# Optimization experiments

Measured on AMD Instinct MI355X. Metric: run time of the kernel, lower is better.

The kernel has to match this reference:

```python
import jax, jax.numpy as jnp
import numpy as np

E = 1024
H = 16
D = E // H  # 64
S = 2048
B = 4


def setup_inputs() -> dict:
    key = jax.random.key(0)
    ks = jax.random.split(key, 9)
    scale = 1.0 / np.sqrt(E)
    inp = {"x": jax.random.normal(ks[0], (S, B, E), dtype=jnp.float32)}
    for i, name in enumerate(["q", "k", "v", "o"]):
        inp[f"W{name}"] = jax.random.uniform(ks[1 + 2 * i], (E, E), dtype=jnp.float32, minval=-scale, maxval=scale)
        inp[f"b{name}"] = jax.random.uniform(ks[2 + 2 * i], (E,), dtype=jnp.float32, minval=-scale, maxval=scale)
    return inp


def reference(x, Wq, bq, Wk, bk, Wv, bv, Wo, bo):
    s, b, e = x.shape
    # linear projections (torch Linear: x @ W.T + b), split into heads
    q = (x @ Wq.T + bq).reshape(s, b, H, D)
    k = (x @ Wk.T + bk).reshape(s, b, H, D)
    v = (x @ Wv.T + bv).reshape(s, b, H, D)
    # naive O(S^2) attention, scores: [S, B, H, S]
    scores = jnp.einsum('sbhd,tbhd->sbht', q, k) / np.sqrt(D).astype(np.float32)
    attn = jax.nn.softmax(scores, axis=3)
    # dropout p=0.0 (eval) -> identity
    out = jnp.einsum('sbht,tbhd->sbhd', attn, v).reshape(s, b, e)
    return out @ Wo.T + bo
```

## Files before the change

### kernel.cpp

```cpp
#include <hip/hip_runtime.h>
#include <hip/hip_bf16.h>

#define S_LEN 2048
#define BATCH 4
#define EMB   1024
#define NH    16
#define HD    64
#define NROW  8192

#define QSCALE 0.18033688011112043f

typedef __bf16 bf16x8 __attribute__((ext_vector_type(8)));
typedef float  f32x4  __attribute__((ext_vector_type(4)));

typedef __attribute__((address_space(3))) void lds_void;
typedef const __attribute__((address_space(1))) void gbl_void;
#define GLOAD_LDS16(g, l) __builtin_amdgcn_global_load_lds((gbl_void*)(g), (lds_void*)(l), 16, 0, 0)
#define MFMA16(a, b, c) __builtin_amdgcn_mfma_f32_16x16x32_bf16((a), (b), (c), 0, 0, 0)

#if __has_builtin(__builtin_amdgcn_exp2f)
#define EXP2(x) __builtin_amdgcn_exp2f(x)
#else
#define EXP2(x) __expf((x) * 0.6931471805599453f)
#endif

__global__ void cvt_all_kernel(const float* __restrict__ x,
                               const float* __restrict__ wq, const float* __restrict__ wk,
                               const float* __restrict__ wv, const float* __restrict__ wo,
                               __bf16* __restrict__ xb,
                               __bf16* __restrict__ qb, __bf16* __restrict__ kb,
                               __bf16* __restrict__ vb, __bf16* __restrict__ ob) {
    const int bid = blockIdx.x;
    const float* src;
    __bf16* dst;
    int i;
    if (bid < 8192) {
        src = x; dst = xb; i = bid * 256 + threadIdx.x;
    } else {
        const int w = (bid - 8192) >> 10;
        src = w == 0 ? wq : (w == 1 ? wk : (w == 2 ? wv : wo));
        dst = w == 0 ? qb : (w == 1 ? kb : (w == 2 ? vb : ob));
        i = ((bid - 8192) & 1023) * 256 + threadIdx.x;
    }
    float4 v = ((const float4*)src)[i];
    union { __bf16 h[4]; short4 s4; } u;
    u.h[0] = (__bf16)v.x; u.h[1] = (__bf16)v.y;
    u.h[2] = (__bf16)v.z; u.h[3] = (__bf16)v.w;
    ((short4*)dst)[i] = u.s4;
}

#define GSTEP(C, BT, VM, DOSTAGE) do {                                        \
    asm volatile("s_waitcnt vmcnt(" VM ")" ::: "memory");                     \
    __builtin_amdgcn_s_barrier();                                             \
    if (DOSTAGE) {                                                            \
        GLOAD_LDS16(gA0 + ((C) + 2) * 32, ldsA + (((BT) + 2) % 3) * 4096);    \
        GLOAD_LDS16(gA1 + ((C) + 2) * 32, ldsA + (((BT) + 2) % 3) * 4096 + 512); \
        GLOAD_LDS16(gW0 + ((C) + 2) * 32, ldsB + (((BT) + 2) % 3) * 4096);    \
        GLOAD_LDS16(gW1 + ((C) + 2) * 32, ldsB + (((BT) + 2) % 3) * 4096 + 512); \
    }                                                                         \
    bf16x8 af[4], bfr[4];                                                     \
    _Pragma("unroll")                                                         \
    for (int tt = 0; tt < 4; ++tt) {                                          \
        af[tt]  = *(const bf16x8*)(Ab + (BT) * 4096 + tt * 512);              \
        bfr[tt] = *(const bf16x8*)(Bb + (BT) * 4096 + tt * 512);              \
    }                                                                         \
    _Pragma("unroll")                                                         \
    for (int i = 0; i < 4; ++i)                                               \
        _Pragma("unroll")                                                     \
        for (int j = 0; j < 4; ++j)                                           \
            acc[i][j] = MFMA16(af[i], bfr[j], acc[i][j]);                     \
} while (0)

__global__ __launch_bounds__(256) void gemm_qkv_kernel(
    const __bf16* __restrict__ A,
    const __bf16* __restrict__ W0, const __bf16* __restrict__ W1,
    const __bf16* __restrict__ W2,
    const float* __restrict__ bi0, const float* __restrict__ bi1,
    const float* __restrict__ bi2,
    __bf16* __restrict__ Qo, __bf16* __restrict__ Ko, __bf16* __restrict__ Vo)
{
    __shared__ __align__(16) char SMEM[49152];
    __bf16* Asb = (__bf16*)SMEM;
    __bf16* Bsb = (__bf16*)(SMEM + 24576);

    const int flat = blockIdx.x;
    const int xcd = flat & 7, slot = flat >> 3;
    const int nB = slot >> 3;
    const int mB = (xcd << 3) | (slot & 7);
    const int which = nB >> 3;
    const __bf16* W = which == 0 ? W0 : (which == 1 ? W1 : W2);
    const float* bias = which == 0 ? bi0 : (which == 1 ? bi1 : bi2);
    __bf16* outb = which == 0 ? Qo : (which == 1 ? Ko : Vo);
    const int m0 = mB * 128;
    const int n0 = (nB & 7) * 128;

    const int lane = threadIdx.x & 63;
    const int wave = threadIdx.x >> 6;
    const int l15 = lane & 15;
    const int quad = lane >> 4;
    const int wm = (wave >> 1) * 64;
    const int wn = (wave & 1) * 64;

    const int c0 = wave * 128 + lane;
    const int c1 = c0 + 64;
    const int ar0 = c0 >> 2, ak0 = (((c0 & 3) ^ ((c0 >> 3) & 3))) * 8;
    const int ar1 = c1 >> 2, ak1 = (((c1 & 3) ^ ((c1 >> 3) & 3))) * 8;

    const __bf16* Ag = A + (size_t)m0 * EMB;
    const __bf16* Wg = W + (size_t)n0 * EMB;

    f32x4 acc[4][4];
#pragma unroll
    for (int i = 0; i < 4; ++i)
#pragma unroll
        for (int j = 0; j < 4; ++j) acc[i][j] = (f32x4){0.f, 0.f, 0.f, 0.f};

    const __bf16* gA0 = Ag + (size_t)ar0 * EMB + ak0;
    const __bf16* gA1 = Ag + (size_t)ar1 * EMB + ak1;
    const __bf16* gW0 = Wg + (size_t)ar0 * EMB + ak0;
    const __bf16* gW1 = Wg + (size_t)ar1 * EMB + ak1;
    __bf16* ldsA = Asb + wave * 1024;
    __bf16* ldsB = Bsb + wave * 1024;

    GLOAD_LDS16(gA0,      ldsA);
    GLOAD_LDS16(gA1,      ldsA + 512);
    GLOAD_LDS16(gW0,      ldsB);
    GLOAD_LDS16(gW1,      ldsB + 512);
    GLOAD_LDS16(gA0 + 32, ldsA + 4096);
    GLOAD_LDS16(gA1 + 32, ldsA + 4096 + 512);
    GLOAD_LDS16(gW0 + 32, ldsB + 4096);
    GLOAD_LDS16(gW1 + 32, ldsB + 4096 + 512);

    const int xr = (l15 >> 1) & 3;
    const __bf16* Ab = Asb + (wm + l15) * 32 + ((quad ^ xr) << 3);
    const __bf16* Bb = Bsb + (wn + l15) * 32 + ((quad ^ xr) << 3);

    for (int g = 0; g < 10; ++g) {
        GSTEP(0, 0, "4", 1);
        GSTEP(1, 1, "4", 1);
        GSTEP(2, 2, "4", 1);
        gA0 += 96; gA1 += 96; gW0 += 96; gW1 += 96;
    }
    GSTEP(0, 0, "4", 0);
    GSTEP(1, 1, "0", 0);

    __syncthreads();
    __bf16* epi = (__bf16*)SMEM + wave * 2304;
    float bv[4];
#pragma unroll
    for (int j = 0; j < 4; ++j) bv[j] = bias[n0 + wn + j * 16 + l15];
    const int hh = (n0 + wn) >> 6;

    if (which != 2) {
#pragma unroll
        for (int p = 0; p < 2; ++p) {
#pragma unroll
            for (int ih = 0; ih < 2; ++ih) {
                const int i = 2 * p + ih;
#pragma unroll
                for (int j = 0; j < 4; ++j)
#pragma unroll
                    for (int r = 0; r < 4; ++r) {
                        float v = acc[i][j][r] + bv[j];
                        if (which == 0) v *= QSCALE;
                        epi[(ih * 16 + quad * 4 + r) * 72 + j * 16 + l15] = (__bf16)v;
                    }
            }
#pragma unroll
            for (int ii = 0; ii < 4; ++ii) {
                const int rl = ii * 8 + (lane >> 3);
                bf16x8 row = *(const bf16x8*)(epi + rl * 72 + (lane & 7) * 8);
                const int m = m0 + wm + p * 32 + rl;
                const int b = m & 3, s = m >> 2;
                *(bf16x8*)(outb + ((size_t)(b * NH + hh) * S_LEN + s) * HD
                           + (lane & 7) * 8) = row;
            }
        }
    } else {
        const int sb = (m0 + wm) >> 2;
#pragma unroll
        for (int p = 0; p < 2; ++p) {
#pragma unroll
            for (int jh = 0; jh < 2; ++jh) {
                const int j = 2 * p + jh;
#pragma unroll
                for (int i = 0; i < 4; ++i)
#pragma unroll
                    for (int r = 0; r < 4; ++r) {
                        float v = acc[i][j][r] + bv[j];
                        epi[(jh * 16 + l15) * 72 + r * 16 + i * 4 + quad] = (__bf16)v;
                    }
            }
#pragma unroll
            for (int ii = 0; ii < 4; ++ii) {
                const int q = lane >> 1;
                bf16x8 row = *(const bf16x8*)(epi + q * 72 + ii * 16 + (lane & 1) * 8);
                const int d = p * 32 + q;
                *(bf16x8*)(outb + ((size_t)(ii * NH + hh) * HD + d) * S_LEN
                           + sb + (lane & 1) * 8) = row;
            }
        }
    }
}

__global__ __launch_bounds__(256) void gemm_out_kernel(
    const __bf16* __restrict__ A, const __bf16* __restrict__ W,
    const float* __restrict__ bias, float* __restrict__ outf)
{
    __shared__ __align__(16) char SMEM[49152];
    __bf16* Asb = (__bf16*)SMEM;
    __bf16* Bsb = (__bf16*)(SMEM + 24576);
    const int flat = blockIdx.x;
    const int xcd = flat & 7, slot = flat >> 3;
    const int nB = slot >> 3;
    const int mB = (xcd << 3) | (slot & 7);
    const int m0 = mB * 128;
    const int n0 = nB * 128;

    const int lane = threadIdx.x & 63;
    const int wave = threadIdx.x >> 6;
    const int l15 = lane & 15;
    const int quad = lane >> 4;
    const int wm = (wave >> 1) * 64;
    const int wn = (wave & 1) * 64;

    const int c0 = wave * 128 + lane;
    const int c1 = c0 + 64;
    const int ar0 = c0 >> 2, ak0 = (((c0 & 3) ^ ((c0 >> 3) & 3))) * 8;
    const int ar1 = c1 >> 2, ak1 = (((c1 & 3) ^ ((c1 >> 3) & 3))) * 8;

    const __bf16* Ag = A + (size_t)m0 * EMB;
    const __bf16* Wg = W + (size_t)n0 * EMB;

    f32x4 acc[4][4];
#pragma unroll
    for (int i = 0; i < 4; ++i)
#pragma unroll
        for (int j = 0; j < 4; ++j) acc[i][j] = (f32x4){0.f, 0.f, 0.f, 0.f};

    const __bf16* gA0 = Ag + (size_t)ar0 * EMB + ak0;
    const __bf16* gA1 = Ag + (size_t)ar1 * EMB + ak1;
    const __bf16* gW0 = Wg + (size_t)ar0 * EMB + ak0;
    const __bf16* gW1 = Wg + (size_t)ar1 * EMB + ak1;
    __bf16* ldsA = Asb + wave * 1024;
    __bf16* ldsB = Bsb + wave * 1024;

    GLOAD_LDS16(gA0,      ldsA);
    GLOAD_LDS16(gA1,      ldsA + 512);
    GLOAD_LDS16(gW0,      ldsB);
    GLOAD_LDS16(gW1,      ldsB + 512);
    GLOAD_LDS16(gA0 + 32, ldsA + 4096);
    GLOAD_LDS16(gA1 + 32, ldsA + 4096 + 512);
    GLOAD_LDS16(gW0 + 32, ldsB + 4096);
    GLOAD_LDS16(gW1 + 32, ldsB + 4096 + 512);

    const int xr = (l15 >> 1) & 3;
    const __bf16* Ab = Asb + (wm + l15) * 32 + ((quad ^ xr) << 3);
    const __bf16* Bb = Bsb + (wn + l15) * 32 + ((quad ^ xr) << 3);

    for (int g = 0; g < 10; ++g) {
        GSTEP(0, 0, "4", 1);
        GSTEP(1, 1, "4", 1);
        GSTEP(2, 2, "4", 1);
        gA0 += 96; gA1 += 96; gW0 += 96; gW1 += 96;
    }
    GSTEP(0, 0, "4", 0);
    GSTEP(1, 1, "0", 0);

#pragma unroll
    for (int j = 0; j < 4; ++j) {
        const int col = n0 + wn + j * 16 + l15;
        const float bv = bias[col];
#pragma unroll
        for (int i = 0; i < 4; ++i)
#pragma unroll
            for (int r = 0; r < 4; ++r) {
                const int m = m0 + wm + i * 16 + quad * 4 + r;
                outf[(size_t)m * EMB + col] = acc[i][j][r] + bv;
            }
    }
}

__global__ __launch_bounds__(256, 4) void attn_kernel(
    const __bf16* __restrict__ Q, const __bf16* __restrict__ Kp,
    const __bf16* __restrict__ Vt, __bf16* __restrict__ Ao)
{
    __shared__ __align__(16) __bf16 Ks[3][32 * 64];
    __shared__ __align__(16) __bf16 Vs[3][32 * 64];

    const int tid = threadIdx.x;
    const int lane = tid & 63;
    const int wave = tid >> 6;
    const int l15 = lane & 15;
    const int quad = lane >> 4;

    const int flat = blockIdx.y * gridDim.x + blockIdx.x;
    const int nf = (flat & 7) * 128 + (flat >> 3);
    const int bh = nf >> 4;
    const int b = bh >> 4, h = bh & 15;
    const int qw = (nf & 15) * 128 + wave * 32;

    const __bf16* Qb = Q  + (size_t)bh * S_LEN * HD;
    const __bf16* Kb = Kp + (size_t)bh * S_LEN * HD;
    const __bf16* Vb = Vt + (size_t)bh * HD * S_LEN;

    const int kr = tid >> 3;
    const int ks = ((tid & 7) ^ ((kr & 3) | (((kr >> 3) & 1) << 2))) * 8;
    const int vr = tid >> 2;
    const int vs = (((tid & 3) ^ ((tid >> 3) & 3))) * 8;

    bf16x8 qf[2][2];
#pragma unroll
    for (int mi = 0; mi < 2; ++mi)
#pragma unroll
        for (int kc = 0; kc < 2; ++kc)
            qf[mi][kc] = *(const bf16x8*)(Qb + (size_t)(qw + mi * 16 + l15) * HD
                                          + kc * 32 + quad * 8);

    bf16x8 ones;
#pragma unroll
    for (int i = 0; i < 8; ++i) ones[i] = (__bf16)1.0f;

    f32x4 acco[2][4], accl[2];
#pragma unroll
    for (int mi = 0; mi < 2; ++mi) {
        accl[mi] = (f32x4){0.f, 0.f, 0.f, 0.f};
#pragma unroll
        for (int nt = 0; nt < 4; ++nt) acco[mi][nt] = (f32x4){0.f, 0.f, 0.f, 0.f};
    }

    auto stageKV = [&](int t) {
        const int t0 = t * 32;
        GLOAD_LDS16(Kb + (size_t)(t0 + kr) * HD + ks, &Ks[t % 3][wave * 512]);
        GLOAD_LDS16(Vb + (size_t)vr * S_LEN + t0 + vs, &Vs[t % 3][wave * 512]);
    };
    stageKV(0);
    stageKV(1);

    const int ta = 8 * (l15 >> 2) + (l15 & 3);
    const int xk = (l15 & 3) | (((l15 >> 2) & 1) << 2);
    const int xv = (l15 >> 1) & 3;

    for (int it = 0; it < S_LEN / 32; ++it) {
        if (it < S_LEN / 32 - 1) asm volatile("s_waitcnt vmcnt(2)" ::: "memory");
        else                     asm volatile("s_waitcnt vmcnt(0)" ::: "memory");
        __builtin_amdgcn_s_barrier();
        if (it + 2 < S_LEN / 32) stageKV(it + 2);

        const __bf16* Kt = &Ks[it % 3][0];
        const __bf16* Vl = &Vs[it % 3][0];

        bf16x8 kfA[2], kfB[2], vf[4];
#pragma unroll
        for (int kc = 0; kc < 2; ++kc) {
            kfA[kc] = *(const bf16x8*)(Kt + ta * 64 + (((kc * 4 + quad) ^ xk) << 3));
            kfB[kc] = *(const bf16x8*)(Kt + (ta + 4) * 64 + (((kc * 4 + quad) ^ xk) << 3));
        }
#pragma unroll
        for (int nt = 0; nt < 4; ++nt)
            vf[nt] = *(const bf16x8*)(Vl + (nt * 16 + l15) * 32 + ((quad ^ xv) << 3));

        bf16x8 pf[2];
#pragma unroll
        for (int mi = 0; mi < 2; ++mi) {
            f32x4 sA = {0.f, 0.f, 0.f, 0.f}, sB = {0.f, 0.f, 0.f, 0.f};
            __builtin_amdgcn_s_setprio(1);
            sA = MFMA16(kfA[0], qf[mi][0], sA);
            sA = MFMA16(kfA[1], qf[mi][1], sA);
            sB = MFMA16(kfB[0], qf[mi][0], sB);
            sB = MFMA16(kfB[1], qf[mi][1], sB);
            __builtin_amdgcn_s_setprio(0);
            union { __bf16 hh[8]; bf16x8 v; } u;
#pragma unroll
            for (int r = 0; r < 4; ++r) {
                u.hh[r]     = (__bf16)EXP2(sA[r]);
                u.hh[4 + r] = (__bf16)EXP2(sB[r]);
            }
            pf[mi] = u.v;
        }
        __builtin_amdgcn_s_setprio(1);
#pragma unroll
        for (int mi = 0; mi < 2; ++mi)
            accl[mi] = MFMA16(pf[mi], ones, accl[mi]);
#pragma unroll
        for (int nt = 0; nt < 4; ++nt)
#pragma unroll
            for (int mi = 0; mi < 2; ++mi)
                acco[mi][nt] = MFMA16(pf[mi], vf[nt], acco[mi][nt]);
        __builtin_amdgcn_s_setprio(0);
    }

#pragma unroll
    for (int mi = 0; mi < 2; ++mi)
#pragma unroll
        for (int r = 0; r < 4; ++r) {
            const float inv = 1.0f / accl[mi][r];
            const int srow = qw + mi * 16 + quad * 4 + r;
            const int n = srow * BATCH + b;
#pragma unroll
            for (int nt = 0; nt < 4; ++nt)
                Ao[(size_t)n * EMB + h * 64 + nt * 16 + l15] =
                    (__bf16)(acco[mi][nt][r] * inv);
        }
}

extern "C" void kernel_launch(void* const* d_in, const int* in_sizes, int n_in,
                              void* d_out, int out_size, void* d_ws, size_t ws_size,
                              hipStream_t stream) {
    const float* x  = (const float*)d_in[0];
    const float* Wq = (const float*)d_in[1];
    const float* bq = (const float*)d_in[2];
    const float* Wk = (const float*)d_in[3];
    const float* bk = (const float*)d_in[4];
    const float* Wv = (const float*)d_in[5];
    const float* bv = (const float*)d_in[6];
    const float* Wo = (const float*)d_in[7];
    const float* bo = (const float*)d_in[8];
    float* out = (float*)d_out;

    char* ws = (char*)d_ws;
    const size_t xbf_sz = (size_t)NROW * EMB * 2;
    const size_t wbf_sz = (size_t)EMB * EMB * 2;
    const size_t qkv_sz = (size_t)BATCH * NH * S_LEN * HD * 2;
    __bf16* x_bf  = (__bf16*)ws;  ws += xbf_sz;
    __bf16* Wq_bf = (__bf16*)ws;  ws += wbf_sz;
    __bf16* Wk_bf = (__bf16*)ws;  ws += wbf_sz;
    __bf16* Wv_bf = (__bf16*)ws;  ws += wbf_sz;
    __bf16* Wo_bf = (__bf16*)ws;  ws += wbf_sz;
    __bf16* Qb    = (__bf16*)ws;  ws += qkv_sz;
    __bf16* Kb    = (__bf16*)ws;  ws += qkv_sz;
    __bf16* Vtb   = (__bf16*)ws;  ws += qkv_sz;
    __bf16* Aob   = (__bf16*)ws;  ws += qkv_sz;

    cvt_all_kernel<<<8192 + 4 * 1024, 256, 0, stream>>>(
        x, Wq, Wk, Wv, Wo, x_bf, Wq_bf, Wk_bf, Wv_bf, Wo_bf);

    gemm_qkv_kernel<<<64 * 24, 256, 0, stream>>>(x_bf, Wq_bf, Wk_bf, Wv_bf,
                                                 bq, bk, bv, Qb, Kb, Vtb);
    dim3 ag(S_LEN / 128, BATCH * NH);
    attn_kernel<<<ag, 256, 0, stream>>>(Qb, Kb, Vtb, Aob);
    gemm_out_kernel<<<(NROW / 128) * (EMB / 128), 256, 0, stream>>>(Aob, Wo_bf, bo, out);
}
```

Baseline: 251.8 us.

## Halve output GEMM M-tile to 64 rows and add LDS sync waits

The output projection GEMM now uses 64x128 tiles instead of 128x128, so the launch grows from 512 to 1024 blocks, each using less LDS and fewer accumulators. The aim is better occupancy and load balance across the CUs. The change also adds lgkmcnt(0) to the pipeline waits in the GEMM and attention loops and a __syncthreads between the two epilogue halves of the QKV kernel, which fixes LDS ordering hazards. In exchange the smaller tile re-reads the weight matrix from memory more often, and each block does less MFMA work per barrier.

```diff
diff --git a/kernel.cpp b/kernel.cpp
--- a/kernel.cpp
+++ b/kernel.cpp
@@ -50,7 +50,7 @@
 }
 
 #define GSTEP(C, BT, VM, DOSTAGE) do {                                        \
-    asm volatile("s_waitcnt vmcnt(" VM ")" ::: "memory");                     \
+    asm volatile("s_waitcnt vmcnt(" VM ") lgkmcnt(0)" ::: "memory");          \
     __builtin_amdgcn_s_barrier();                                             \
     if (DOSTAGE) {                                                            \
         GLOAD_LDS16(gA0 + ((C) + 2) * 32, ldsA + (((BT) + 2) % 3) * 4096);    \
@@ -71,6 +71,28 @@
             acc[i][j] = MFMA16(af[i], bfr[j], acc[i][j]);                     \
 } while (0)
 
+#define GSTEP2(C, BT, VM, DOSTAGE) do {                                       \
+    asm volatile("s_waitcnt vmcnt(" VM ") lgkmcnt(0)" ::: "memory");          \
+    __builtin_amdgcn_s_barrier();                                             \
+    if (DOSTAGE) {                                                            \
+        GLOAD_LDS16(gA0 + ((C) + 2) * 32, ldsA + (((BT) + 2) % 3) * 2048);    \
+        GLOAD_LDS16(gW0 + ((C) + 2) * 32, ldsB + (((BT) + 2) % 3) * 4096);    \
+        GLOAD_LDS16(gW1 + ((C) + 2) * 32, ldsB + (((BT) + 2) % 3) * 4096 + 512); \
+    }                                                                         \
+    bf16x8 af[2], bfr[4];                                                     \
+    _Pragma("unroll")                                                         \
+    for (int tt = 0; tt < 2; ++tt)                                            \
+        af[tt] = *(const bf16x8*)(Ab + (BT) * 2048 + tt * 512);               \
+    _Pragma("unroll")                                                         \
+    for (int tt = 0; tt < 4; ++tt)                                            \
+        bfr[tt] = *(const bf16x8*)(Bb + (BT) * 4096 + tt * 512);              \
+    _Pragma("unroll")                                                         \
+    for (int i = 0; i < 2; ++i)                                               \
+        _Pragma("unroll")                                                     \
+        for (int j = 0; j < 4; ++j)                                           \
+            acc[i][j] = MFMA16(af[i], bfr[j], acc[i][j]);                     \
+} while (0)
+
 __global__ __launch_bounds__(256) void gemm_qkv_kernel(
     const __bf16* __restrict__ A,
     const __bf16* __restrict__ W0, const __bf16* __restrict__ W1,
@@ -175,6 +197,7 @@
                 *(bf16x8*)(outb + ((size_t)(b * NH + hh) * S_LEN + s) * HD
                            + (lane & 7) * 8) = row;
             }
+            if (p == 0) __syncthreads();
         }
     } else {
         const int sb = (m0 + wm) >> 2;
@@ -199,6 +222,7 @@
                 *(bf16x8*)(outb + ((size_t)(ii * NH + hh) * HD + d) * S_LEN
                            + sb + (lane & 1) * 8) = row;
             }
+            if (p == 0) __syncthreads();
         }
     }
 }
@@ -207,50 +231,47 @@
     const __bf16* __restrict__ A, const __bf16* __restrict__ W,
     const float* __restrict__ bias, float* __restrict__ outf)
 {
-    __shared__ __align__(16) char SMEM[49152];
+    __shared__ __align__(16) char SMEM[36864];
     __bf16* Asb = (__bf16*)SMEM;
-    __bf16* Bsb = (__bf16*)(SMEM + 24576);
+    __bf16* Bsb = (__bf16*)(SMEM + 12288);
+
+    const int tid = threadIdx.x;
     const int flat = blockIdx.x;
     const int xcd = flat & 7, slot = flat >> 3;
-    const int nB = slot >> 3;
-    const int mB = (xcd << 3) | (slot & 7);
-    const int m0 = mB * 128;
+    const int nB = slot >> 4;
+    const int mB = (xcd << 4) | (slot & 15);
+    const int m0 = mB * 64;
     const int n0 = nB * 128;
 
-    const int lane = threadIdx.x & 63;
-    const int wave = threadIdx.x >> 6;
+    const int lane = tid & 63;
+    const int wave = tid >> 6;
     const int l15 = lane & 15;
     const int quad = lane >> 4;
-    const int wm = (wave >> 1) * 64;
+    const int wm = (wave >> 1) * 32;
     const int wn = (wave & 1) * 64;
 
+    const int ar = tid >> 2, aak = (((tid & 3) ^ ((tid >> 3) & 3))) * 8;
     const int c0 = wave * 128 + lane;
     const int c1 = c0 + 64;
-    const int ar0 = c0 >> 2, ak0 = (((c0 & 3) ^ ((c0 >> 3) & 3))) * 8;
-    const int ar1 = c1 >> 2, ak1 = (((c1 & 3) ^ ((c1 >> 3) & 3))) * 8;
-
-    const __bf16* Ag = A + (size_t)m0 * EMB;
-    const __bf16* Wg = W + (size_t)n0 * EMB;
-
-    f32x4 acc[4][4];
-#pragma unroll
-    for (int i = 0; i < 4; ++i)
+    const int br0 = c0 >> 2, bk0 = (((c0 & 3) ^ ((c0 >> 3) & 3))) * 8;
+    const int br1 = c1 >> 2, bk1 = (((c1 & 3) ^ ((c1 >> 3) & 3))) * 8;
+
+    const __bf16* gA0 = A + (size_t)(m0 + ar) * EMB + aak;
+    const __bf16* gW0 = W + (size_t)(n0 + br0) * EMB + bk0;
+    const __bf16* gW1 = W + (size_t)(n0 + br1) * EMB + bk1;
+    __bf16* ldsA = Asb + wave * 512;
+    __bf16* ldsB = Bsb + wave * 1024;
+
+    f32x4 acc[2][4];
+#pragma unroll
+    for (int i = 0; i < 2; ++i)
 #pragma unroll
         for (int j = 0; j < 4; ++j) acc[i][j] = (f32x4){0.f, 0.f, 0.f, 0.f};
 
-    const __bf16* gA0 = Ag + (size_t)ar0 * EMB + ak0;
-    const __bf16* gA1 = Ag + (size_t)ar1 * EMB + ak1;
-    const __bf16* gW0 = Wg + (size_t)ar0 * EMB + ak0;
-    const __bf16* gW1 = Wg + (size_t)ar1 * EMB + ak1;
-    __bf16* ldsA = Asb + wave * 1024;
-    __bf16* ldsB = Bsb + wave * 1024;
-
     GLOAD_LDS16(gA0,      ldsA);
-    GLOAD_LDS16(gA1,      ldsA + 512);
     GLOAD_LDS16(gW0,      ldsB);
     GLOAD_LDS16(gW1,      ldsB + 512);
-    GLOAD_LDS16(gA0 + 32, ldsA + 4096);
-    GLOAD_LDS16(gA1 + 32, ldsA + 4096 + 512);
+    GLOAD_LDS16(gA0 + 32, ldsA + 2048);
     GLOAD_LDS16(gW0 + 32, ldsB + 4096);
     GLOAD_LDS16(gW1 + 32, ldsB + 4096 + 512);
 
@@ -259,20 +280,20 @@
     const __bf16* Bb = Bsb + (wn + l15) * 32 + ((quad ^ xr) << 3);
 
     for (int g = 0; g < 10; ++g) {
-        GSTEP(0, 0, "4", 1);
-        GSTEP(1, 1, "4", 1);
-        GSTEP(2, 2, "4", 1);
-        gA0 += 96; gA1 += 96; gW0 += 96; gW1 += 96;
-    }
-    GSTEP(0, 0, "4", 0);
-    GSTEP(1, 1, "0", 0);
+        GSTEP2(0, 0, "3", 1);
+        GSTEP2(1, 1, "3", 1);
+        GSTEP2(2, 2, "3", 1);
+        gA0 += 96; gW0 += 96; gW1 += 96;
+    }
+    GSTEP2(0, 0, "3", 0);
+    GSTEP2(1, 1, "0", 0);
 
 #pragma unroll
     for (int j = 0; j < 4; ++j) {
         const int col = n0 + wn + j * 16 + l15;
         const float bv = bias[col];
 #pragma unroll
-        for (int i = 0; i < 4; ++i)
+        for (int i = 0; i < 2; ++i)
 #pragma unroll
             for (int r = 0; r < 4; ++r) {
                 const int m = m0 + wm + i * 16 + quad * 4 + r;
@@ -342,8 +363,8 @@
     const int xv = (l15 >> 1) & 3;
 
     for (int it = 0; it < S_LEN / 32; ++it) {
-        if (it < S_LEN / 32 - 1) asm volatile("s_waitcnt vmcnt(2)" ::: "memory");
-        else                     asm volatile("s_waitcnt vmcnt(0)" ::: "memory");
+        if (it < S_LEN / 32 - 1) asm volatile("s_waitcnt vmcnt(2) lgkmcnt(0)" ::: "memory");
+        else                     asm volatile("s_waitcnt vmcnt(0) lgkmcnt(0)" ::: "memory");
         __builtin_amdgcn_s_barrier();
         if (it + 2 < S_LEN / 32) stageKV(it + 2);
 
@@ -439,5 +460,5 @@
                                                  bq, bk, bv, Qb, Kb, Vtb);
     dim3 ag(S_LEN / 128, BATCH * NH);
     attn_kernel<<<ag, 256, 0, stream>>>(Qb, Kb, Vtb, Aob);
-    gemm_out_kernel<<<(NROW / 128) * (EMB / 128), 256, 0, stream>>>(Aob, Wo_bf, bo, out);
+    gemm_out_kernel<<<1024, 256, 0, stream>>>(Aob, Wo_bf, bo, out);
 }
```

Result: no change. 255.2 us (+1.4%).
